# Optimization experiments

Hardware: AMD Instinct MI355X
Metric: run time of the kernel (lower is better)

The kernel has to match this reference:

```python
import jax, jax.numpy as jnp
import numpy as np

D_MODEL = 2048
EXPAND = 2
D_INNER = EXPAND * D_MODEL   # 4096
D_STATE = 128
D_CONV = 4
HEADDIM = 64
NHEADS = D_INNER // HEADDIM  # 64
NGROUPS = 1
CONV_DIM = D_INNER + 2 * NGROUPS * D_STATE           # 4352
D_IN_PROJ = 2 * D_INNER + 2 * NGROUPS * D_STATE + NHEADS  # 8512
B, T = 2, 2048
EPS = 1e-5


def setup_inputs() -> dict:
    key = jax.random.key(0)
    ks = jax.random.split(key, 12)
    x = jax.random.normal(ks[0], (B, T, D_MODEL), dtype=jnp.float32)
    cos = jax.random.normal(ks[1], (T, HEADDIM), dtype=jnp.float32)
    sin = jax.random.normal(ks[2], (T, HEADDIM), dtype=jnp.float32)
    in_proj_w = jax.random.normal(ks[3], (D_IN_PROJ, D_MODEL), dtype=jnp.float32) * 0.02
    conv_w = jax.random.normal(ks[4], (CONV_DIM, D_CONV), dtype=jnp.float32) * 0.2
    conv_b = jnp.zeros((CONV_DIM,), dtype=jnp.float32)
    # dt_bias = softplus^{-1}(dt) for dt ~ U[0.001, 0.1]
    dt = jax.random.uniform(ks[5], (NHEADS,), minval=0.001, maxval=0.1)
    dt_bias = (jnp.log(jnp.expm1(dt))).astype(jnp.float32)
    A_log = jnp.log(jax.random.uniform(ks[6], (NHEADS,), minval=1.0, maxval=16.0)).astype(jnp.float32)
    Dskip = jnp.ones((NHEADS,), dtype=jnp.float32)
    norm_w = jnp.ones((D_INNER,), dtype=jnp.float32)
    out_proj_w = jax.random.normal(ks[7], (D_MODEL, D_INNER), dtype=jnp.float32) * 0.02
    return {"x": x, "cos": cos, "sin": sin, "in_proj_w": in_proj_w,
            "conv_w": conv_w, "conv_b": conv_b, "dt_bias": dt_bias,
            "A_log": A_log, "Dskip": Dskip, "norm_w": norm_w,
            "out_proj_w": out_proj_w}


def _mamba2_fwd(x, in_proj_w, conv_w, conv_b, dt_bias, A_log, Dskip, norm_w, out_proj_w):
    # in_proj -> [z, xBC, dt]
    zxbcdt = jnp.einsum('btd,ed->bte', x, in_proj_w)  # [B,T,8512]
    z = zxbcdt[..., :D_INNER]
    xBC = zxbcdt[..., D_INNER:D_INNER + CONV_DIM]
    dt_raw = zxbcdt[..., D_INNER + CONV_DIM:]          # [B,T,H]

    # depthwise causal conv1d + SiLU
    xBC_pad = jnp.pad(xBC, ((0, 0), (D_CONV - 1, 0), (0, 0)))
    conv = conv_b
    for k in range(D_CONV):
        conv = conv + xBC_pad[:, k:k + T, :] * conv_w[:, k]
    xBC = jax.nn.silu(conv)

    x_ssm = xBC[..., :D_INNER].reshape(x.shape[0], T, NHEADS, HEADDIM)  # [B,T,H,P]
    Bmat = xBC[..., D_INNER:D_INNER + D_STATE]                          # [B,T,N] (ngroups=1)
    Cmat = xBC[..., D_INNER + D_STATE:]                                 # [B,T,N]

    dt = jax.nn.softplus(dt_raw + dt_bias)   # [B,T,H]
    A = -jnp.exp(A_log)                      # [H]
    dA = jnp.exp(dt * A)                     # [B,T,H], in (0,1]
    dtx = dt[..., None] * x_ssm              # [B,T,H,P]

    # selective scan over time (state h: [B,H,P,N])
    def step(h, xs_t):
        dA_t, dtx_t, B_t, C_t = xs_t  # [B,H],[B,H,P],[B,N],[B,N]
        h = h * dA_t[:, :, None, None] + dtx_t[:, :, :, None] * B_t[:, None, None, :]
        y = jnp.einsum('bhpn,bn->bhp', h, C_t)
        return h, y

    h0 = jnp.zeros((x.shape[0], NHEADS, HEADDIM, D_STATE), dtype=x.dtype)
    xs = (jnp.swapaxes(dA, 0, 1), jnp.swapaxes(dtx, 0, 1),
          jnp.swapaxes(Bmat, 0, 1), jnp.swapaxes(Cmat, 0, 1))
    _, ys = jax.lax.scan(step, h0, xs)       # ys: [T,B,H,P]
    y = jnp.swapaxes(ys, 0, 1) + Dskip[None, None, :, None] * x_ssm  # [B,T,H,P]
    y = y.reshape(x.shape[0], T, D_INNER)

    # gated RMSNorm: gate first, then normalize
    y = y * jax.nn.silu(z)
    y = y * jax.lax.rsqrt(jnp.mean(jnp.square(y), axis=-1, keepdims=True) + EPS) * norm_w

    return jnp.einsum('bte,de->btd', y, out_proj_w)  # [B,T,D]


def reference(x, cos, sin, in_proj_w, conv_w, conv_b, dt_bias, A_log, Dskip, norm_w, out_proj_w):
    # cos/sin accepted but ignored (Mamba needs no positional encoding)
    return _mamba2_fwd(x, in_proj_w, conv_w, conv_b, dt_bias, A_log, Dskip, norm_w, out_proj_w)
```

## Files before the change

kernel.cpp:

```cpp
#include <hip/hip_runtime.h>

#define D_MODEL 2048
#define D_INNER 4096
#define D_STATE 128
#define HEADDIM 64
#define NHEADS 64
#define CONV_DIM 4352
#define D_IN_PROJ 8512
#define BB 2
#define TSEQ 2048
#define BT (BB*TSEQ)
#define NCHUNK 32
#define LCH 64
#define EPS_F 1e-5f

typedef __bf16 bf16x8 __attribute__((ext_vector_type(8)));
typedef float f32x4 __attribute__((ext_vector_type(4)));

__device__ __forceinline__ float bf2f(unsigned short u){
  unsigned int x = ((unsigned int)u) << 16;
  return __builtin_bit_cast(float, x);
}
__device__ __forceinline__ unsigned short f2bf(float f){
  unsigned int x = __builtin_bit_cast(unsigned int, f);
  x += 0x7fffu + ((x >> 16) & 1u);
  return (unsigned short)(x >> 16);
}

__device__ __forceinline__ void async_copy16(const unsigned short* g, unsigned short* l) {
  __builtin_amdgcn_global_load_lds(
      (const __attribute__((address_space(1))) unsigned int*)g,
      (__attribute__((address_space(3))) unsigned int*)l, 16, 0, 0);
}

__global__ __launch_bounds__(256) void cast_kernel(
    const float* __restrict__ in, unsigned short* __restrict__ out, int n)
{
  int i = (blockIdx.x * 256 + threadIdx.x) * 8;
  if (i >= n) return;
  float4 a = *(const float4*)&in[i];
  float4 b = *(const float4*)&in[i + 4];
  unsigned short o[8] = { f2bf(a.x), f2bf(a.y), f2bf(a.z), f2bf(a.w),
                          f2bf(b.x), f2bf(b.y), f2bf(b.z), f2bf(b.w) };
  *(uint4*)&out[i] = *(uint4*)o;
}

template <bool F32OUT>
__global__ __launch_bounds__(512, 2) void gemm256_kernel(
    const unsigned short* __restrict__ A, const unsigned short* __restrict__ Bm,
    void* __restrict__ Cout, int M, int N, int K, int NT, int MT)
{
  __shared__ __align__(16) unsigned short As[4][256 * 32];
  __shared__ __align__(16) unsigned short Bs[4][256 * 32];
  int tid = threadIdx.x;

  int bid = blockIdx.x;
  int fullBands = NT >> 3;
  int blocksFull = fullBands * 8 * MT;
  int mt, nt;
  if (bid < blocksFull) {
    int band = bid / (8 * MT);
    int wI = bid - band * (8 * MT);
    nt = band * 8 + (wI & 7);
    mt = wI >> 3;
  } else {
    int rem = bid - blocksFull;
    int WL = NT - fullBands * 8;
    nt = fullBands * 8 + rem % WL;
    mt = rem / WL;
  }
  int m0 = mt * 256, n0 = nt * 256;

  int wid = tid >> 6, lane = tid & 63;
  int wm = wid >> 2, wn = wid & 3;
  int lm = lane & 15, kqb = lane >> 4;
  int rsw = (kqb ^ ((lm >> 1) & 3)) * 8;

  int srow = tid >> 2;
  int sblk = (tid & 3) ^ ((srow >> 1) & 3);
  const unsigned short* Ap = A + (size_t)(m0 + srow) * K + sblk * 8;
  const unsigned short* Bp = Bm + (size_t)(n0 + srow) * K + sblk * 8;

  f32x4 acc[8][4] = {};
  const int U = K >> 5;

#pragma unroll
  for (int u = 0; u < 3; u++) {
    int ku = u << 5;
    async_copy16(Ap + ku, &As[u][wid * 512]);
    async_copy16(Ap + (size_t)128 * K + ku, &As[u][4096 + wid * 512]);
    async_copy16(Bp + ku, &Bs[u][wid * 512]);
    async_copy16(Bp + (size_t)128 * K + ku, &Bs[u][4096 + wid * 512]);
  }

  for (int u = 0; u < U; u++) {
    int s = u & 3;
    int left = U - 1 - u;
    if (left >= 2)      asm volatile("s_waitcnt vmcnt(8)" ::: "memory");
    else if (left == 1) asm volatile("s_waitcnt vmcnt(4)" ::: "memory");
    else                asm volatile("s_waitcnt vmcnt(0)" ::: "memory");
    __builtin_amdgcn_s_barrier();

    const unsigned short* Ab = &As[s][wm * 4096];
    const unsigned short* Bb = &Bs[s][(wn * 64) * 32];
    int up = u + 3;
    int kup = up << 5, sp = up & 3;

    bf16x8 bfr[4], af[4];
#pragma unroll
    for (int j = 0; j < 4; j++) bfr[j] = *(const bf16x8*)&Bb[(j * 16 + lm) * 32 + rsw];
#pragma unroll
    for (int i = 0; i < 4; i++) af[i] = *(const bf16x8*)&Ab[(i * 16 + lm) * 32 + rsw];
    if (up < U) {
      async_copy16(Ap + kup, &As[sp][wid * 512]);
      async_copy16(Ap + (size_t)128 * K + kup, &As[sp][4096 + wid * 512]);
    }
    __builtin_amdgcn_s_setprio(1);
#pragma unroll
    for (int i = 0; i < 4; i++)
#pragma unroll
      for (int j = 0; j < 4; j++)
        acc[i][j] = __builtin_amdgcn_mfma_f32_16x16x32_bf16(af[i], bfr[j], acc[i][j], 0, 0, 0);
    __builtin_amdgcn_s_setprio(0);
    __builtin_amdgcn_s_barrier();

#pragma unroll
    for (int i = 0; i < 4; i++) af[i] = *(const bf16x8*)&Ab[((4 + i) * 16 + lm) * 32 + rsw];
    if (up < U) {
      async_copy16(Bp + kup, &Bs[sp][wid * 512]);
      async_copy16(Bp + (size_t)128 * K + kup, &Bs[sp][4096 + wid * 512]);
    }
    __builtin_amdgcn_s_setprio(1);
#pragma unroll
    for (int i = 0; i < 4; i++)
#pragma unroll
      for (int j = 0; j < 4; j++)
        acc[4 + i][j] = __builtin_amdgcn_mfma_f32_16x16x32_bf16(af[i], bfr[j], acc[4 + i][j], 0, 0, 0);
    __builtin_amdgcn_s_setprio(0);
  }

  int rq = lane >> 4;
#pragma unroll
  for (int i = 0; i < 8; i++) {
#pragma unroll
    for (int j = 0; j < 4; j++) {
      int col = n0 + wn * 64 + j * 16 + lm;
      if (col < N) {
        int mrow = m0 + wm * 128 + i * 16 + rq * 4;
#pragma unroll
        for (int r = 0; r < 4; r++) {
          if (F32OUT) ((float*)Cout)[(size_t)(mrow + r) * N + col] = acc[i][j][r];
          else ((unsigned short*)Cout)[(size_t)(mrow + r) * N + col] = f2bf(acc[i][j][r]);
        }
      }
    }
  }
}

template <bool F32OUT>
__global__ __launch_bounds__(256) void gemm_tn_kernel(
    const unsigned short* __restrict__ A, const unsigned short* __restrict__ Bm,
    void* __restrict__ Cout, int M, int N, int K, int NT, int MT)
{
  __shared__ __align__(16) unsigned short As[128 * 64];
  __shared__ __align__(16) unsigned short Bs[128 * 64];
  int tid = threadIdx.x;

  int bid = blockIdx.x;
  int fullBands = NT >> 3;
  int blocksFull = fullBands * 8 * MT;
  int mt, nt;
  if (bid < blocksFull) {
    int band = bid / (8 * MT);
    int wI = bid - band * (8 * MT);
    nt = band * 8 + (wI & 7);
    mt = wI >> 3;
  } else {
    int rem = bid - blocksFull;
    int WL = NT - fullBands * 8;
    nt = fullBands * 8 + rem % WL;
    mt = rem / WL;
  }
  int m0 = mt * 128, n0 = nt * 128;

  int wave = tid >> 6, lane = tid & 63;
  int wm = wave >> 1, wn = wave & 1;
  int lm = lane & 15, kqb = lane >> 4;
  int sw = lm & 7;

  int lr = lane >> 3, lc = lane & 7, bg = lc ^ lr;
  const unsigned short* Ap = A + (size_t)(m0 + wave * 32 + lr) * K + bg * 8;
  const unsigned short* Bp = Bm + (size_t)(n0 + wave * 32 + lr) * K + bg * 8;

  f32x4 acc[4][4] = {};

  for (int k0 = 0; k0 < K; k0 += 64) {
#pragma unroll
    for (int q = 0; q < 4; q++) {
      async_copy16(Ap + (size_t)q * 8 * K + k0, &As[(wave * 32 + q * 8) * 64]);
      async_copy16(Bp + (size_t)q * 8 * K + k0, &Bs[(wave * 32 + q * 8) * 64]);
    }
    __syncthreads();
#pragma unroll
    for (int kk = 0; kk < 64; kk += 32) {
      int b0 = (kk >> 3) + kqb;
      int boff = (b0 ^ sw) * 8;
      bf16x8 af[4], bfr[4];
#pragma unroll
      for (int i = 0; i < 4; i++) af[i]  = *(const bf16x8*)&As[(wm * 64 + i * 16 + lm) * 64 + boff];
#pragma unroll
      for (int j = 0; j < 4; j++) bfr[j] = *(const bf16x8*)&Bs[(wn * 64 + j * 16 + lm) * 64 + boff];
#pragma unroll
      for (int i = 0; i < 4; i++)
#pragma unroll
        for (int j = 0; j < 4; j++)
          acc[i][j] = __builtin_amdgcn_mfma_f32_16x16x32_bf16(af[i], bfr[j], acc[i][j], 0, 0, 0);
    }
    __syncthreads();
  }

  int rq = lane >> 4;
#pragma unroll
  for (int i = 0; i < 4; i++) {
#pragma unroll
    for (int j = 0; j < 4; j++) {
      int col = n0 + wn * 64 + j * 16 + lm;
      if (col < N) {
        int mrow = m0 + wm * 64 + i * 16 + rq * 4;
#pragma unroll
        for (int r = 0; r < 4; r++) {
          if (F32OUT) ((float*)Cout)[(size_t)(mrow + r) * N + col] = acc[i][j][r];
          else ((unsigned short*)Cout)[(size_t)(mrow + r) * N + col] = f2bf(acc[i][j][r]);
        }
      }
    }
  }
}

__global__ __launch_bounds__(256) void conv_silu_kernel(
    const unsigned short* __restrict__ zx, const float* __restrict__ conv_w,
    const float* __restrict__ conv_b, unsigned short* __restrict__ xconv,
    unsigned short* __restrict__ Bbf, unsigned short* __restrict__ Cbf)
{
  const int NG = CONV_DIM / 8;
  int gid = blockIdx.x * 256 + threadIdx.x;
  if (gid >= BT * NG) return;
  int cg = gid % NG; int bt = gid / NG;
  int t = bt % TSEQ;
  int c0 = cg * 8;

  float wgt[8][4];
#pragma unroll
  for (int i = 0; i < 8; i++)
#pragma unroll
    for (int k = 0; k < 4; k++) wgt[i][k] = conv_w[(c0 + i) * 4 + k];

  float acc[8];
#pragma unroll
  for (int i = 0; i < 8; i++) acc[i] = conv_b[c0 + i];

#pragma unroll
  for (int k = 0; k < 4; k++) {
    int ts = t - 3 + k;
    if (ts < 0) continue;
    unsigned short xv[8];
    *(uint4*)xv = *(const uint4*)&zx[(size_t)(bt - 3 + k) * D_IN_PROJ + D_INNER + c0];
#pragma unroll
    for (int i = 0; i < 8; i++) acc[i] = fmaf(bf2f(xv[i]), wgt[i][k], acc[i]);
  }

  unsigned short o[8];
#pragma unroll
  for (int i = 0; i < 8; i++) { float v = acc[i]; o[i] = f2bf(v / (1.f + expf(-v))); }
  if (c0 < D_INNER) {
    *(uint4*)&xconv[(size_t)bt * D_INNER + c0] = *(uint4*)o;
  } else if (c0 < D_INNER + D_STATE) {
    *(uint4*)&Bbf[(size_t)bt * D_STATE + (c0 - D_INNER)] = *(uint4*)o;
  } else {
    *(uint4*)&Cbf[(size_t)bt * D_STATE + (c0 - D_INNER - D_STATE)] = *(uint4*)o;
  }
}

__global__ __launch_bounds__(256) void dtcum_kernel(
    const unsigned short* __restrict__ zx, const float* __restrict__ dt_bias,
    const float* __restrict__ A_log, float* __restrict__ dtv, float* __restrict__ ca)
{
  int g = blockIdx.x * 4 + (threadIdx.x >> 6);
  int lane = threadIdx.x & 63;
  int h = g & 63; int cb = g >> 6;
  size_t bt = (size_t)cb * 64 + lane;
  float xr = bf2f(zx[bt * D_IN_PROJ + D_INNER + CONV_DIM + h]) + dt_bias[h];
  float dt = (xr > 20.f) ? xr : log1pf(expf(xr));
  float v = dt * (-expf(A_log[h]));
#pragma unroll
  for (int off = 1; off < 64; off <<= 1) {
    float t = __shfl_up(v, off);
    if (lane >= off) v += t;
  }
  dtv[bt * NHEADS + h] = dt;
  ca[(size_t)g * 64 + lane] = v;
}

__global__ __launch_bounds__(256) void chunk_g_kernel(
    const unsigned short* __restrict__ Bbf, const unsigned short* __restrict__ Cbf,
    unsigned short* __restrict__ G)
{
  __shared__ __align__(16) unsigned short Cs[64][136];
  __shared__ __align__(16) unsigned short Bs2[64][136];
  int tid = threadIdx.x; int cb = blockIdx.x;
  size_t bt0 = (size_t)cb * 64;
  int row = tid >> 2, seg = (tid & 3) * 32;
#pragma unroll
  for (int u = 0; u < 32; u += 8) {
    *(uint4*)&Cs[row][seg + u]  = *(const uint4*)&Cbf[(bt0 + row) * 128 + seg + u];
    *(uint4*)&Bs2[row][seg + u] = *(const uint4*)&Bbf[(bt0 + row) * 128 + seg + u];
  }
  __syncthreads();
  int wave = tid >> 6, lane = tid & 63, lm = lane & 15, kq = (lane >> 4) * 8, rq = lane >> 4;
  f32x4 acc[4] = {};
#pragma unroll
  for (int ks = 0; ks < 4; ks++) {
    bf16x8 af = *(const bf16x8*)&Cs[wave * 16 + lm][ks * 32 + kq];
#pragma unroll
    for (int jt = 0; jt < 4; jt++) {
      bf16x8 bb = *(const bf16x8*)&Bs2[jt * 16 + lm][ks * 32 + kq];
      acc[jt] = __builtin_amdgcn_mfma_f32_16x16x32_bf16(af, bb, acc[jt], 0, 0, 0);
    }
  }
#pragma unroll
  for (int jt = 0; jt < 4; jt++)
#pragma unroll
    for (int r = 0; r < 4; r++) {
      int i = wave * 16 + rq * 4 + r, j = jt * 16 + lm;
      G[(size_t)cb * 4096 + i * 64 + j] = f2bf(acc[jt][r]);
    }
}

__global__ __launch_bounds__(256) void chunk_state_kernel(
    const unsigned short* __restrict__ Bbf, const unsigned short* __restrict__ xconv,
    const float* __restrict__ dtv, const float* __restrict__ ca,
    unsigned short* __restrict__ S)
{
  __shared__ __align__(16) unsigned short Ax[64][72];
  __shared__ __align__(16) unsigned short Bn[128][72];
  int tid = threadIdx.x;
  int c = blockIdx.x & 31, hb = (blockIdx.x >> 5) & 15, b = blockIdx.x >> 9;
  int cb = b * 32 + c;
  size_t bt0 = (size_t)cb * 64;
  {
    int j = tid >> 2, nseg = (tid & 3) * 32;
    unsigned short bv[32];
#pragma unroll
    for (int u = 0; u < 32; u += 8)
      *(uint4*)&bv[u] = *(const uint4*)&Bbf[(bt0 + j) * 128 + nseg + u];
#pragma unroll
    for (int u = 0; u < 32; u++) Bn[nseg + u][j] = bv[u];
  }
  int wave = tid >> 6, lane = tid & 63, lm = lane & 15, kq = (lane >> 4) * 8, rq = lane >> 4;
  int j = tid >> 2, pseg = (tid & 3) * 16;
  for (int hh = 0; hh < 4; hh++) {
    int h = hb * 4 + hh;
    const float* cag = &ca[((size_t)cb * 64 + h) * 64];
    float wj = expf(cag[63] - cag[j]) * dtv[(bt0 + j) * 64 + h];
    unsigned short xv[16];
    *(uint4*)&xv[0] = *(const uint4*)&xconv[(bt0 + j) * 4096 + h * 64 + pseg];
    *(uint4*)&xv[8] = *(const uint4*)&xconv[(bt0 + j) * 4096 + h * 64 + pseg + 8];
    if (hh) __syncthreads();
#pragma unroll
    for (int q = 0; q < 16; q++) Ax[pseg + q][j] = f2bf(wj * bf2f(xv[q]));
    __syncthreads();
    f32x4 acc[8] = {};
#pragma unroll
    for (int ks = 0; ks < 2; ks++) {
      bf16x8 af = *(const bf16x8*)&Ax[wave * 16 + lm][ks * 32 + kq];
#pragma unroll
      for (int nt = 0; nt < 8; nt++) {
        bf16x8 bb = *(const bf16x8*)&Bn[nt * 16 + lm][ks * 32 + kq];
        acc[nt] = __builtin_amdgcn_mfma_f32_16x16x32_bf16(af, bb, acc[nt], 0, 0, 0);
      }
    }
    size_t sbase = ((size_t)(b * 64 + h) * 32 + c) * 8192;
#pragma unroll
    for (int nt = 0; nt < 8; nt++)
#pragma unroll
      for (int r = 0; r < 4; r++) {
        int p = wave * 16 + rq * 4 + r, n = nt * 16 + lm;
        S[sbase + p * 128 + n] = f2bf(acc[nt][r]);
      }
  }
}

__global__ __launch_bounds__(256) void state_pass_kernel(
    unsigned short* __restrict__ Shin, const float* __restrict__ ca)
{
  int part = blockIdx.x & 7, bh = blockIdx.x >> 3;
  int h = bh & 63, b = bh >> 6;
  int e0 = part * 1024 + threadIdx.x * 4;
  size_t base = (size_t)bh * 32 * 8192;
  float hc[4] = {0.f, 0.f, 0.f, 0.f};
  for (int c = 0; c < 32; c++) {
    float sc = expf(ca[(((size_t)(b * 32 + c)) * 64 + h) * 64 + 63]);
    size_t off = base + (size_t)c * 8192 + e0;
    uint2 sv = *(uint2*)&Shin[off];
    unsigned short* sp = (unsigned short*)&sv;
    unsigned short ho[4];
#pragma unroll
    for (int q = 0; q < 4; q++) ho[q] = f2bf(hc[q]);
    *(uint2*)&Shin[off] = *(uint2*)ho;
#pragma unroll
    for (int q = 0; q < 4; q++) hc[q] = sc * hc[q] + bf2f(sp[q]);
  }
}

__global__ __launch_bounds__(256) void chunk_y_kernel(
    const unsigned short* __restrict__ G, const unsigned short* __restrict__ Cbf,
    const unsigned short* __restrict__ xconv, const float* __restrict__ dtv,
    const float* __restrict__ ca, const unsigned short* __restrict__ hin,
    const float* __restrict__ Dskip, unsigned short* __restrict__ yp)
{
  __shared__ __align__(16) unsigned short Aop[64][200];
  __shared__ __align__(16) unsigned short Bop[64][200];
  __shared__ float cas[64]; __shared__ float dts[64];
  int tid = threadIdx.x;
  int c = blockIdx.x & 31, h = (blockIdx.x >> 5) & 63, b = blockIdx.x >> 11;
  int cb = b * 32 + c;
  size_t bt0 = (size_t)cb * 64;
  if (tid < 64) {
    cas[tid] = ca[((size_t)cb * 64 + h) * 64 + tid];
    dts[tid] = dtv[(bt0 + tid) * 64 + h];
  }
  __syncthreads();
  {
    int i = tid >> 2, jseg = (tid & 3) * 16;
    float cai = cas[i];
    unsigned short gv[16];
    *(uint4*)&gv[0] = *(const uint4*)&G[(size_t)cb * 4096 + i * 64 + jseg];
    *(uint4*)&gv[8] = *(const uint4*)&G[(size_t)cb * 4096 + i * 64 + jseg + 8];
    unsigned short o[16];
#pragma unroll
    for (int q = 0; q < 16; q++) {
      int j = jseg + q;
      float m = (j <= i) ? bf2f(gv[q]) * expf(cai - cas[j]) * dts[j] : 0.f;
      o[q] = f2bf(m);
    }
    *(uint4*)&Aop[i][jseg] = *(uint4*)&o[0];
    *(uint4*)&Aop[i][jseg + 8] = *(uint4*)&o[8];
  }
  {
    int i = tid >> 2, nseg = (tid & 3) * 32;
    float sci = expf(cas[i]);
#pragma unroll
    for (int u = 0; u < 32; u += 8) {
      unsigned short cv[8];
      *(uint4*)cv = *(const uint4*)&Cbf[(bt0 + i) * 128 + nseg + u];
      unsigned short o[8];
#pragma unroll
      for (int q = 0; q < 8; q++) o[q] = f2bf(sci * bf2f(cv[q]));
      *(uint4*)&Aop[i][64 + nseg + u] = *(uint4*)o;
    }
  }
  {
    int j = tid >> 2, pseg = (tid & 3) * 16;
    unsigned short xv[16];
    *(uint4*)&xv[0] = *(const uint4*)&xconv[(bt0 + j) * 4096 + h * 64 + pseg];
    *(uint4*)&xv[8] = *(const uint4*)&xconv[(bt0 + j) * 4096 + h * 64 + pseg + 8];
#pragma unroll
    for (int q = 0; q < 16; q++) Bop[pseg + q][j] = xv[q];
  }
  {
    int p = tid >> 2, nseg = (tid & 3) * 32;
    size_t hb = ((size_t)(b * 64 + h) * 32 + c) * 8192 + p * 128 + nseg;
#pragma unroll
    for (int u = 0; u < 32; u += 8)
      *(uint4*)&Bop[p][64 + nseg + u] = *(const uint4*)&hin[hb + u];
  }
  __syncthreads();
  int wave = tid >> 6, lane = tid & 63, lm = lane & 15, kq = (lane >> 4) * 8, rq = lane >> 4;
  f32x4 acc[4] = {};
#pragma unroll
  for (int ks = 0; ks < 6; ks++) {
    bf16x8 af = *(const bf16x8*)&Aop[wave * 16 + lm][ks * 32 + kq];
#pragma unroll
    for (int pt = 0; pt < 4; pt++) {
      bf16x8 bb = *(const bf16x8*)&Bop[pt * 16 + lm][ks * 32 + kq];
      acc[pt] = __builtin_amdgcn_mfma_f32_16x16x32_bf16(af, bb, acc[pt], 0, 0, 0);
    }
  }
  float dsk = Dskip[h];
#pragma unroll
  for (int pt = 0; pt < 4; pt++)
#pragma unroll
    for (int r = 0; r < 4; r++) {
      int i = wave * 16 + rq * 4 + r, p = pt * 16 + lm;
      float y = acc[pt][r] + dsk * bf2f(Bop[p][i]);
      yp[(bt0 + i) * 4096 + h * 64 + p] = f2bf(y);
    }
}

__global__ __launch_bounds__(256) void gate_norm_kernel(
    const unsigned short* __restrict__ yp, const unsigned short* __restrict__ zx,
    const float* __restrict__ norm_w, unsigned short* __restrict__ ybf)
{
  int row = blockIdx.x; int tid = threadIdx.x;
  int c0 = tid * 16;
  unsigned short y0[16], zv[16];
  const size_t base = (size_t)row * D_INNER + c0;
  *(uint4*)&y0[0] = *(const uint4*)&yp[base];
  *(uint4*)&y0[8] = *(const uint4*)&yp[base + 8];
  const size_t zbase = (size_t)row * D_IN_PROJ + c0;
  *(uint4*)&zv[0] = *(const uint4*)&zx[zbase];
  *(uint4*)&zv[8] = *(const uint4*)&zx[zbase + 8];

  float g[16]; float ss = 0.f;
#pragma unroll
  for (int i = 0; i < 16; i++) {
    float y = bf2f(y0[i]);
    float z = bf2f(zv[i]);
    float gate = z / (1.f + expf(-z));
    float gv = y * gate;
    g[i] = gv; ss += gv * gv;
  }
#pragma unroll
  for (int o = 32; o >= 1; o >>= 1) ss += __shfl_xor(ss, o);
  __shared__ float red[4]; __shared__ float stot;
  if ((tid & 63) == 0) red[tid >> 6] = ss;
  __syncthreads();
  if (tid == 0) stot = red[0] + red[1] + red[2] + red[3];
  __syncthreads();
  float scale = rsqrtf(stot * (1.f / D_INNER) + EPS_F);
  unsigned short o16[16];
#pragma unroll
  for (int i = 0; i < 16; i++) o16[i] = f2bf(g[i] * scale * norm_w[c0 + i]);
  *(uint4*)&ybf[base] = *(uint4*)&o16[0];
  *(uint4*)&ybf[base + 8] = *(uint4*)&o16[8];
}

extern "C" void kernel_launch(void* const* d_in, const int* in_sizes, int n_in,
                              void* d_out, int out_size, void* d_ws, size_t ws_size,
                              hipStream_t stream) {
  (void)in_sizes; (void)n_in; (void)out_size; (void)ws_size;
  const float* x          = (const float*)d_in[0];
  const float* in_proj_w  = (const float*)d_in[3];
  const float* conv_w     = (const float*)d_in[4];
  const float* conv_b     = (const float*)d_in[5];
  const float* dt_bias    = (const float*)d_in[6];
  const float* A_log      = (const float*)d_in[7];
  const float* Dskip      = (const float*)d_in[8];
  const float* norm_w     = (const float*)d_in[9];
  const float* out_proj_w = (const float*)d_in[10];
  float* out = (float*)d_out;

  char* w = (char*)d_ws;
  unsigned short* zx    = (unsigned short*)(w);
  unsigned short* xconv = (unsigned short*)(w + 69730304);
  unsigned short* Bbf = (unsigned short*)(w + 103284736);
  unsigned short* Cbf = (unsigned short*)(w + 105381888);
  float* dtv = (float*)(w + 107479040);
  float* ca  = (float*)(w + 109576192);
  unsigned short* G    = (unsigned short*)(w + 110624768);
  unsigned short* Shin = (unsigned short*)(w + 111149056);
  unsigned short* yp   = (unsigned short*)(w + 178257920);
  unsigned short* xb   = (unsigned short*)(w + 111149056);
  unsigned short* wib  = (unsigned short*)(w + 127926272);
  unsigned short* ybf  = (unsigned short*)(w + 111149056);
  unsigned short* wob  = (unsigned short*)(w + 144703488);

  cast_kernel<<<BT * D_MODEL / 8 / 256, 256, 0, stream>>>(x, xb, BT * D_MODEL);
  cast_kernel<<<D_IN_PROJ * D_MODEL / 8 / 256, 256, 0, stream>>>(in_proj_w, wib, D_IN_PROJ * D_MODEL);
  {
    int NT = 34, MT = BT / 256;
    gemm256_kernel<false><<<NT * MT, 512, 0, stream>>>(
        xb, wib, zx, BT, D_IN_PROJ, D_MODEL, NT, MT);
  }
  conv_silu_kernel<<<(BT * (CONV_DIM / 8) + 255) / 256, 256, 0, stream>>>(
      zx, conv_w, conv_b, xconv, Bbf, Cbf);
  dtcum_kernel<<<BB * NCHUNK * NHEADS / 4, 256, 0, stream>>>(zx, dt_bias, A_log, dtv, ca);
  chunk_g_kernel<<<BB * NCHUNK, 256, 0, stream>>>(Bbf, Cbf, G);
  chunk_state_kernel<<<BB * 16 * NCHUNK, 256, 0, stream>>>(Bbf, xconv, dtv, ca, Shin);
  state_pass_kernel<<<BB * NHEADS * 8, 256, 0, stream>>>(Shin, ca);
  chunk_y_kernel<<<BB * NHEADS * NCHUNK, 256, 0, stream>>>(G, Cbf, xconv, dtv, ca, Shin, Dskip, yp);
  gate_norm_kernel<<<BT, 256, 0, stream>>>(yp, zx, norm_w, ybf);
  cast_kernel<<<D_MODEL * D_INNER / 8 / 256, 256, 0, stream>>>(out_proj_w, wob, D_MODEL * D_INNER);
  {
    int NT = D_MODEL / 128, MT = BT / 128;
    gemm_tn_kernel<true><<<NT * MT, 256, 0, stream>>>(
        ybf, wob, out, BT, D_MODEL, D_INNER, NT, MT);
  }
}
```

Before: 612.5 us.

## Software-pipeline LDS fragment loads across GEMM k-steps with register double buffering

Restructures the bf16 GEMM main loop so the A/B fragments for the next k-step are read from LDS right after the barrier, while the second half of the current step's MFMAs is still pending. The loop is unrolled by two, swapping two register fragment sets. The vmcnt waits are retuned for the new position of the barrier. This aims to hide LDS read latency behind MFMA work, at the cost of more live VGPRs. The loop also assumes U is even, and the waitcnt logic must stay correct so no stage is read before its copy lands.

```diff
diff --git a/kernel.cpp b/kernel.cpp
--- a/kernel.cpp
+++ b/kernel.cpp
@@ -44,6 +44,60 @@
                           f2bf(b.x), f2bf(b.y), f2bf(b.z), f2bf(b.w) };
   *(uint4*)&out[i] = *(uint4*)o;
 }
+
+#define GUNIT(u_, CA, CB, NA, NB)                                              \
+  {                                                                            \
+    const int s_ = (u_) & 3;                                                   \
+    const int up_ = (u_) + 3;                                                  \
+    const unsigned short* Ab_ = &As[s_][wm * 4096];                            \
+    _Pragma("unroll")                                                          \
+    for (int i = 0; i < 4; i++)                                                \
+      aD[i] = *(const bf16x8*)&Ab_[((4 + i) * 16 + lm) * 32 + rsw];            \
+    if (up_ < U) {                                                             \
+      int kup_ = up_ << 5; int sp_ = up_ & 3;                                  \
+      async_copy16(Ap + kup_, &As[sp_][wid * 512]);                            \
+      async_copy16(Ap + (size_t)128 * K + kup_, &As[sp_][4096 + wid * 512]);   \
+    }                                                                          \
+    __builtin_amdgcn_s_setprio(1);                                             \
+    _Pragma("unroll")                                                          \
+    for (int i = 0; i < 4; i++)                                                \
+      _Pragma("unroll")                                                        \
+      for (int j = 0; j < 4; j++)                                              \
+        acc[i][j] = __builtin_amdgcn_mfma_f32_16x16x32_bf16(                   \
+            CA[i], CB[j], acc[i][j], 0, 0, 0);                                 \
+    __builtin_amdgcn_s_setprio(0);                                             \
+    {                                                                          \
+      int left_ = U - 1 - (u_);                                                \
+      if (left_ >= 3)      asm volatile("s_waitcnt vmcnt(6)" ::: "memory");    \
+      else if (left_ == 2) asm volatile("s_waitcnt vmcnt(4)" ::: "memory");    \
+      else                 asm volatile("s_waitcnt vmcnt(0)" ::: "memory");    \
+    }                                                                          \
+    __builtin_amdgcn_s_barrier();                                              \
+    if ((u_) + 1 < U) {                                                        \
+      const int sn_ = ((u_) + 1) & 3;                                          \
+      const unsigned short* Abn_ = &As[sn_][wm * 4096];                        \
+      const unsigned short* Bbn_ = &Bs[sn_][(wn * 64) * 32];                   \
+      _Pragma("unroll")                                                        \
+      for (int j = 0; j < 4; j++)                                              \
+        NB[j] = *(const bf16x8*)&Bbn_[(j * 16 + lm) * 32 + rsw];               \
+      _Pragma("unroll")                                                        \
+      for (int i = 0; i < 4; i++)                                              \
+        NA[i] = *(const bf16x8*)&Abn_[(i * 16 + lm) * 32 + rsw];               \
+    }                                                                          \
+    if (up_ < U) {                                                             \
+      int kup_ = up_ << 5; int sp_ = up_ & 3;                                  \
+      async_copy16(Bp + kup_, &Bs[sp_][wid * 512]);                            \
+      async_copy16(Bp + (size_t)128 * K + kup_, &Bs[sp_][4096 + wid * 512]);   \
+    }                                                                          \
+    __builtin_amdgcn_s_setprio(1);                                             \
+    _Pragma("unroll")                                                          \
+    for (int i = 0; i < 4; i++)                                                \
+      _Pragma("unroll")                                                        \
+      for (int j = 0; j < 4; j++)                                              \
+        acc[4 + i][j] = __builtin_amdgcn_mfma_f32_16x16x32_bf16(               \
+            aD[i], CB[j], acc[4 + i][j], 0, 0, 0);                             \
+    __builtin_amdgcn_s_setprio(0);                                             \
+  }
 
 template <bool F32OUT>
 __global__ __launch_bounds__(512, 2) void gemm256_kernel(
@@ -93,50 +147,22 @@
     async_copy16(Bp + (size_t)128 * K + ku, &Bs[u][4096 + wid * 512]);
   }
 
-  for (int u = 0; u < U; u++) {
-    int s = u & 3;
-    int left = U - 1 - u;
-    if (left >= 2)      asm volatile("s_waitcnt vmcnt(8)" ::: "memory");
-    else if (left == 1) asm volatile("s_waitcnt vmcnt(4)" ::: "memory");
-    else                asm volatile("s_waitcnt vmcnt(0)" ::: "memory");
-    __builtin_amdgcn_s_barrier();
-
-    const unsigned short* Ab = &As[s][wm * 4096];
-    const unsigned short* Bb = &Bs[s][(wn * 64) * 32];
-    int up = u + 3;
-    int kup = up << 5, sp = up & 3;
-
-    bf16x8 bfr[4], af[4];
-#pragma unroll
-    for (int j = 0; j < 4; j++) bfr[j] = *(const bf16x8*)&Bb[(j * 16 + lm) * 32 + rsw];
-#pragma unroll
-    for (int i = 0; i < 4; i++) af[i] = *(const bf16x8*)&Ab[(i * 16 + lm) * 32 + rsw];
-    if (up < U) {
-      async_copy16(Ap + kup, &As[sp][wid * 512]);
-      async_copy16(Ap + (size_t)128 * K + kup, &As[sp][4096 + wid * 512]);
-    }
-    __builtin_amdgcn_s_setprio(1);
-#pragma unroll
-    for (int i = 0; i < 4; i++)
-#pragma unroll
-      for (int j = 0; j < 4; j++)
-        acc[i][j] = __builtin_amdgcn_mfma_f32_16x16x32_bf16(af[i], bfr[j], acc[i][j], 0, 0, 0);
-    __builtin_amdgcn_s_setprio(0);
-    __builtin_amdgcn_s_barrier();
-
-#pragma unroll
-    for (int i = 0; i < 4; i++) af[i] = *(const bf16x8*)&Ab[((4 + i) * 16 + lm) * 32 + rsw];
-    if (up < U) {
-      async_copy16(Bp + kup, &Bs[sp][wid * 512]);
-      async_copy16(Bp + (size_t)128 * K + kup, &Bs[sp][4096 + wid * 512]);
-    }
-    __builtin_amdgcn_s_setprio(1);
-#pragma unroll
-    for (int i = 0; i < 4; i++)
-#pragma unroll
-      for (int j = 0; j < 4; j++)
-        acc[4 + i][j] = __builtin_amdgcn_mfma_f32_16x16x32_bf16(af[i], bfr[j], acc[4 + i][j], 0, 0, 0);
-    __builtin_amdgcn_s_setprio(0);
+  bf16x8 aC[4], bC[4], aN[4], bN[4], aD[4];
+
+  asm volatile("s_waitcnt vmcnt(8)" ::: "memory");
+  __builtin_amdgcn_s_barrier();
+  {
+    const unsigned short* Ab0 = &As[0][wm * 4096];
+    const unsigned short* Bb0 = &Bs[0][(wn * 64) * 32];
+#pragma unroll
+    for (int j = 0; j < 4; j++) bC[j] = *(const bf16x8*)&Bb0[(j * 16 + lm) * 32 + rsw];
+#pragma unroll
+    for (int i = 0; i < 4; i++) aC[i] = *(const bf16x8*)&Ab0[(i * 16 + lm) * 32 + rsw];
+  }
+
+  for (int u = 0; u < U; u += 2) {
+    GUNIT(u,     aC, bC, aN, bN);
+    GUNIT(u + 1, aN, bN, aC, bC);
   }
 
   int rq = lane >> 4;
```

Result: no change. 602.6 us (-1.6%).
